# Performance work log

Hardware: AMD Instinct MI355X
Metric: run time of the kernel (lower is better)

Reference implementation:

```python
import jax, jax.numpy as jnp
import numpy as np

B, N, H = 32, 1024, 512
THR = 0.05  # peak_detection_threshold


def _l2norm(x):
    return x / jnp.linalg.norm(x, axis=-1, keepdims=True)


def setup_inputs() -> dict:
    key = jax.random.key(0)
    ks = jax.random.split(key, 6)
    def w(k, shape, fan_in):
        return jax.random.normal(k, shape, jnp.float32) / np.float32(np.sqrt(fan_in))
    return {
        "segment_rep": jax.random.normal(ks[0], (B, N, H), jnp.float32),
        "phn_mask": jnp.ones((B, N), jnp.float32),
        # SegmentSimilarityMeasure: Linear(2H->H), ReLU, Linear(H->1, no bias)
        "W1": w(ks[1], (2 * H, H), 2 * H),
        "b1": jnp.zeros((H,), jnp.float32),
        "W2": w(ks[2], (H, 1), H),
        # word_enc: Linear(H->H), ReLU, Linear(H->H)
        "We1": w(ks[3], (H, H), H),
        "be1": jnp.zeros((H,), jnp.float32),
        "We2": w(ks[4], (H, H), H),
        "be2": jnp.zeros((H,), jnp.float32),
    }


def _forward(segment_rep, phn_mask, W1, b1, W2, We1, be1, We2, be2):
    Bs, Np, Hd = segment_rep.shape
    # adjacent segment similarity: MLP on concat of l2-normalized neighbors -> (B, N-1)
    cat = jnp.concatenate([_l2norm(segment_rep[:, :-1, :]), _l2norm(segment_rep[:, 1:, :])], axis=2)
    S = (jax.nn.relu(cat @ W1 + b1) @ W2)[..., 0]

    # relative dissimilarity
    Smin = jnp.min(S, axis=1, keepdims=True)
    Smax = jnp.max(S, axis=1, keepdims=True)
    D = 1.0 - (S - Smin) / (Smax - Smin)

    # peak detector (faithful to original, incl. final overwrite of first-order cols -2:)
    z = jnp.zeros_like(D)
    fo = z
    fo = fo.at[:, 0].set(jnp.maximum(D[:, 0] - D[:, 1], 0.0))
    fo = fo.at[:, 1:-1].set(jnp.minimum(jnp.maximum(D[:, 1:-1] - D[:, :-2], 0.0),
                                        jnp.maximum(D[:, 1:-1] - D[:, 2:], 0.0)))
    fo = fo.at[:, -1].set(jnp.maximum(D[:, -1] - D[:, -2], 0.0))
    so = z
    so = so.at[:, 0:2].set(jnp.maximum(D[:, 0:2] - D[:, 2:4], 0.0))
    so = so.at[:, 2:-2].set(jnp.minimum(jnp.maximum(D[:, 2:-2] - D[:, :-4], 0.0),
                                        jnp.maximum(D[:, 2:-2] - D[:, 4:], 0.0)))
    fo = fo.at[:, -2:].set(jnp.maximum(D[:, -2:] - D[:, -4:-2], 0.0))  # replicates original code
    P = jnp.minimum(jnp.maximum(jnp.maximum(fo, so) - THR, 0.0), fo)

    # pad, mask, straight-through hard boundaries
    P = jnp.pad(P, ((0, 0), (0, 1)))
    P = jax.nn.relu(P + (phn_mask - 1.0))
    b_soft = jnp.tanh(10.0 * P)
    b_hard = jnp.tanh(100000.0 * P)
    b = b_soft + jax.lax.stop_gradient(b_hard - b_soft)
    b = jnp.cumsum(b, axis=1)  # (B, N)
    b = b + (b[:, :1] == 0).astype(b.dtype)  # per-row +1 if b[:,0]==0
    num_word_segments = b[:, -1].astype(jnp.int32) + 1  # (B,)

    # U: column j holds j+1 for j < num_word_segments[i], else -100000. Nmax = N (static bound).
    cols = jnp.arange(1, Np + 1, dtype=jnp.int32)  # (Nmax,)
    U = jnp.where(cols[None, :] <= num_word_segments[:, None],
                  cols.astype(segment_rep.dtype)[None, :], -100000.0)  # (B, Nmax)

    V = U[:, None, :] - b[:, :, None]  # (B, N, Nmax)
    Wseg = 1.0 - jnp.tanh(100000.0 * jnp.abs(V))
    Wseg = Wseg / jnp.sum(Wseg, axis=1, keepdims=True)
    Wseg = jnp.nan_to_num(Wseg)

    # pool: (B, Nmax, N) @ (B, N, H) -> (B, Nmax, H)
    word_rep = jnp.einsum('bnm,bnh->bmh', Wseg, segment_rep)
    word_masks = jnp.where(word_rep == 0, 0.0, 1.0)
    out = jax.nn.relu(word_rep @ We1 + be1) @ We2 + be2
    return out * word_masks


def reference(segment_rep, phn_mask, W1, b1, W2, We1, be1, We2, be2):
    return _forward(segment_rep, phn_mask, W1, b1, W2, We1, be1, We2, be2)
```

## Files before the change

kernel.cpp:

```cpp
#include <hip/hip_runtime.h>

#define BB 32
#define NN 1024
#define HH 512
#define NS 1023

typedef unsigned short u16;
typedef unsigned int   u32;
typedef __attribute__((ext_vector_type(8))) short bf16x8;
typedef __attribute__((ext_vector_type(4))) float f32x4;

__device__ __forceinline__ float bf2f(u16 h) {
  union { u32 u; float f; } c; c.u = ((u32)h) << 16; return c.f;
}
__device__ __forceinline__ u16 f2bf(float f) {
  union { float f; u32 u; } c; c.f = f;
  u32 u = c.u;
  return (u16)((u + 0x7fffu + ((u >> 16) & 1u)) >> 16);
}
__device__ __forceinline__ void split_bf(float x, u16& hi, u16& lo) {
  hi = f2bf(x);
  lo = f2bf(x - bf2f(hi));
}
__device__ __forceinline__ void dma16(const u16* g, u16* l) {
  __builtin_amdgcn_global_load_lds(
      (const __attribute__((address_space(1))) u32*)g,
      (__attribute__((address_space(3))) u32*)l, 16, 0, 0);
}

__global__ __launch_bounds__(64) void k_prep_a(const float* __restrict__ seg,
                                               u16* __restrict__ ahi,
                                               u16* __restrict__ alo) {
  int row = blockIdx.x, lane = threadIdx.x;
  const float4* p = (const float4*)(seg + ((size_t)row << 9) + lane * 8);
  float4 a = p[0], b = p[1];
  float v[8] = {a.x, a.y, a.z, a.w, b.x, b.y, b.z, b.w};
  float s = 0.f;
#pragma unroll
  for (int i = 0; i < 8; ++i) s += v[i] * v[i];
#pragma unroll
  for (int m = 32; m; m >>= 1) s += __shfl_xor(s, m, 64);
  float nrm = sqrtf(s);
  u16 h[8], l[8];
#pragma unroll
  for (int i = 0; i < 8; ++i) split_bf(v[i] / nrm, h[i], l[i]);
  size_t off = ((size_t)row << 9) + lane * 8;
  *(uint4*)(ahi + off) = make_uint4(h[0] | (h[1] << 16), h[2] | (h[3] << 16),
                                    h[4] | (h[5] << 16), h[6] | (h[7] << 16));
  *(uint4*)(alo + off) = make_uint4(l[0] | (l[1] << 16), l[2] | (l[3] << 16),
                                    l[4] | (l[5] << 16), l[6] | (l[7] << 16));
}

__global__ __launch_bounds__(256) void k_tr(const float* __restrict__ src,
                                            u16* __restrict__ dh,
                                            u16* __restrict__ dl,
                                            int K, int N) {
  __shared__ u16 Th[64 * 66], Tl[64 * 66];
  int nb = blockIdx.x * 64, kb = blockIdx.y * 64;
  int tid = threadIdx.x;
#pragma unroll
  for (int i = 0; i < 16; ++i) {
    int e = tid + i * 256;
    int r = e >> 6, c = e & 63;
    float v = src[(size_t)(kb + r) * N + nb + c];
    u16 hi, lo; split_bf(v, hi, lo);
    Th[c * 66 + r] = hi;
    Tl[c * 66 + r] = lo;
  }
  __syncthreads();
#pragma unroll
  for (int i = 0; i < 16; ++i) {
    int e = tid + i * 256;
    int n = e >> 6, k = e & 63;
    dh[(size_t)(nb + n) * K + kb + k] = Th[n * 66 + k];
    if (dl) dl[(size_t)(nb + n) * K + kb + k] = Tl[n * 66 + k];
  }
}

__global__ __launch_bounds__(256) void k_sgemm(const u16* __restrict__ ahi,
                                               const u16* __restrict__ alo,
                                               const u16* __restrict__ w1h,
                                               const u16* __restrict__ w1l,
                                               const float* __restrict__ b1,
                                               const float* __restrict__ W2,
                                               float* __restrict__ Spart) {
  __shared__ u16 Ah[2][64 * 32], Al_[2][64 * 32];
  __shared__ u16 Wh[2][256 * 32], Wl[2][256 * 32];

  int tid = threadIdx.x;
  int wave = tid >> 6, lane = tid & 63, quad = lane >> 4, l15 = lane & 15;
  int b = blockIdx.z, mblk = blockIdx.y, nblk = blockIdx.x;
  int rowbase = b * NN + mblk * 64;
  int ncol0 = nblk * 256;
  int r_in = lane >> 2, c_in = lane & 3;

  f32x4 acc[4][4];
#pragma unroll
  for (int mi = 0; mi < 4; ++mi)
#pragma unroll
    for (int ni = 0; ni < 4; ++ni) acc[mi][ni] = (f32x4){0.f, 0.f, 0.f, 0.f};

#define STAGE_TILE(ks_, tb_)                                                        \
  {                                                                                 \
    int k0_ = (ks_) * 32, half_ = k0_ >> 9, cb_ = k0_ & 511;                        \
    int grow_ = rowbase + wave * 16 + r_in + half_;                                 \
    if (grow_ > 32767) grow_ = 32767;                                               \
    size_t ga_ = (((size_t)grow_) << 9) + cb_ + c_in * 8;                           \
    dma16(ahi + ga_, &Ah [tb_][(wave * 16) * 32]);                                  \
    dma16(alo + ga_, &Al_[tb_][(wave * 16) * 32]);                                  \
    _Pragma("unroll")                                                               \
    for (int c_ = 0; c_ < 4; ++c_) {                                                \
      int n_ = wave * 64 + c_ * 16 + r_in;                                          \
      size_t gw_ = (size_t)(ncol0 + n_) * 1024 + k0_ + c_in * 8;                    \
      dma16(w1h + gw_, &Wh[tb_][(wave * 64 + c_ * 16) * 32]);                       \
      dma16(w1l + gw_, &Wl[tb_][(wave * 64 + c_ * 16) * 32]);                       \
    }                                                                               \
  }

  STAGE_TILE(0, 0)
  __syncthreads();

  for (int ks = 0; ks < 32; ++ks) {
    int bb = ks & 1;
    if (ks + 1 < 32) STAGE_TILE(ks + 1, bb ^ 1)

    bf16x8 a_h[4], a_l[4];
#pragma unroll
    for (int mi = 0; mi < 4; ++mi) {
      int off = (mi * 16 + l15) * 32 + quad * 8;
      a_h[mi] = *(const bf16x8*)&Ah [bb][off];
      a_l[mi] = *(const bf16x8*)&Al_[bb][off];
    }
#pragma unroll
    for (int ni = 0; ni < 4; ++ni) {
      int off = (wave * 64 + ni * 16 + l15) * 32 + quad * 8;
      bf16x8 b_h = *(const bf16x8*)&Wh[bb][off];
      bf16x8 b_l = *(const bf16x8*)&Wl[bb][off];
#pragma unroll
      for (int mi = 0; mi < 4; ++mi) {
        acc[mi][ni] = __builtin_amdgcn_mfma_f32_16x16x32_bf16(a_h[mi], b_h, acc[mi][ni], 0, 0, 0);
        acc[mi][ni] = __builtin_amdgcn_mfma_f32_16x16x32_bf16(a_h[mi], b_l, acc[mi][ni], 0, 0, 0);
        acc[mi][ni] = __builtin_amdgcn_mfma_f32_16x16x32_bf16(a_l[mi], b_h, acc[mi][ni], 0, 0, 0);
      }
    }
    __syncthreads();
  }
#undef STAGE_TILE

  float* red = (float*)Ah;
#pragma unroll
  for (int mi = 0; mi < 4; ++mi) {
#pragma unroll
    for (int reg = 0; reg < 4; ++reg) {
      float part = 0.f;
#pragma unroll
      for (int ni = 0; ni < 4; ++ni) {
        int n_g = ncol0 + wave * 64 + ni * 16 + l15;
        float h = acc[mi][ni][reg] + b1[n_g];
        h = h > 0.f ? h : 0.f;
        part = fmaf(h, W2[n_g], part);
      }
#pragma unroll
      for (int m = 8; m; m >>= 1) part += __shfl_xor(part, m, 64);
      if (l15 == 0) red[wave * 64 + mi * 16 + quad * 4 + reg] = part;
    }
  }
  __syncthreads();
  if (tid < 64) {
    float s = red[0 * 64 + tid] + red[1 * 64 + tid] + red[2 * 64 + tid] + red[3 * 64 + tid];
    int srow = mblk * 64 + tid;
    if (srow < NS)
      Spart[((size_t)nblk * BB + b) * NN + srow] = s;
  }
}

__global__ __launch_bounds__(256) void k_row(const float* __restrict__ S0,
                                             const float* __restrict__ S1,
                                             const float* __restrict__ mask,
                                             int* __restrict__ assign,
                                             float* __restrict__ weight,
                                             float* __restrict__ total,
                                             int* __restrict__ startn,
                                             int* __restrict__ endn) {
  int b = blockIdx.x, tid = threadIdx.x;
  __shared__ float Ssh[NS];
  __shared__ float Dsh[NS];
  __shared__ float tsh[NN];
  __shared__ float bsh[NN];
  __shared__ float totl[NN];
  __shared__ int   stl[NN];
  __shared__ int   enl[NN];
  __shared__ float red[256];

  for (int n = tid; n < NS; n += 256)
    Ssh[n] = S0[((size_t)b << 10) + n] + S1[((size_t)b << 10) + n];
  __syncthreads();

  float mn = INFINITY, mx = -INFINITY;
  for (int n = tid; n < NS; n += 256) {
    float v = Ssh[n];
    mn = fminf(mn, v); mx = fmaxf(mx, v);
  }
  red[tid] = mn; __syncthreads();
  for (int s = 128; s; s >>= 1) { if (tid < s) red[tid] = fminf(red[tid], red[tid + s]); __syncthreads(); }
  float Smin = red[0]; __syncthreads();
  red[tid] = mx; __syncthreads();
  for (int s = 128; s; s >>= 1) { if (tid < s) red[tid] = fmaxf(red[tid], red[tid + s]); __syncthreads(); }
  float Smax = red[0]; __syncthreads();

  for (int n = tid; n < NS; n += 256)
    Dsh[n] = 1.0f - (Ssh[n] - Smin) / (Smax - Smin);
  __syncthreads();

  for (int n = tid; n < NN; n += 256) {
    float P;
    if (n >= NS) {
      P = 0.f;
    } else {
      float D = Dsh[n];
      float fo, so;
      if (n == 0)            fo = fmaxf(D - Dsh[1], 0.f);
      else if (n >= NS - 2)  fo = fmaxf(D - Dsh[n - 2], 0.f);
      else                   fo = fminf(fmaxf(D - Dsh[n - 1], 0.f),
                                        fmaxf(D - Dsh[n + 1], 0.f));
      if (n <= 1)            so = fmaxf(D - Dsh[n + 2], 0.f);
      else if (n >= NS - 2)  so = 0.f;
      else                   so = fminf(fmaxf(D - Dsh[n - 2], 0.f),
                                        fmaxf(D - Dsh[n + 2], 0.f));
      P = fminf(fmaxf(fmaxf(fo, so) - 0.05f, 0.f), fo);
    }
    float m = mask[((size_t)b << 10) + n];
    P = P + (m - 1.0f);
    P = P > 0.f ? P : 0.f;
    float bs = tanhf(10.0f * P);
    float bh = tanhf(100000.0f * P);
    tsh[n] = bs + (bh - bs);
  }
  __syncthreads();

  if (tid == 0) {
    float acc = 0.f;
    for (int n = 0; n < NN; n += 8) {
      float t0 = tsh[n + 0], t1 = tsh[n + 1], t2 = tsh[n + 2], t3 = tsh[n + 3];
      float t4 = tsh[n + 4], t5 = tsh[n + 5], t6 = tsh[n + 6], t7 = tsh[n + 7];
      acc += t0; bsh[n + 0] = acc; acc += t1; bsh[n + 1] = acc;
      acc += t2; bsh[n + 2] = acc; acc += t3; bsh[n + 3] = acc;
      acc += t4; bsh[n + 4] = acc; acc += t5; bsh[n + 5] = acc;
      acc += t6; bsh[n + 6] = acc; acc += t7; bsh[n + 7] = acc;
    }
  }
  __syncthreads();

  float add1 = (bsh[0] == 0.0f) ? 1.0f : 0.0f;
  int   num  = (int)(bsh[NN - 1] + add1) + 1;

  for (int mi = tid; mi < NN; mi += 256) { totl[mi] = 0.f; stl[mi] = 1 << 30; enl[mi] = -1; }
  __syncthreads();

  for (int n = tid; n < NN; n += 256) {
    float bv = bsh[n] + add1;
    float kf = rintf(bv);
    int   k  = (int)kf;
    int   a  = -1; float w = 0.f;
    if (k >= 1 && k <= num && k <= NN) {
      float v = fabsf(kf - bv);
      w = 1.0f - tanhf(100000.0f * v);
      if (w > 0.f) {
        a = k - 1;
        atomicAdd(&totl[a], w);
        atomicMin(&stl[a], n);
        atomicMax(&enl[a], n);
      } else {
        a = -1; w = 0.f;
      }
    }
    assign[((size_t)b << 10) + n] = a;
    weight[((size_t)b << 10) + n] = w;
  }
  __syncthreads();
  for (int mi = tid; mi < NN; mi += 256) {
    total [((size_t)b << 10) + mi] = totl[mi];
    startn[((size_t)b << 10) + mi] = stl[mi];
    endn  [((size_t)b << 10) + mi] = enl[mi];
  }
}

__global__ __launch_bounds__(64) void k_pool(const float* __restrict__ seg,
                                             const int* __restrict__ assign,
                                             const float* __restrict__ weight,
                                             const float* __restrict__ total,
                                             const int* __restrict__ startn,
                                             const int* __restrict__ endn,
                                             float* __restrict__ wrep) {
  int bm = blockIdx.x;
  int b  = bm >> 10, m = bm & 1023;
  int lane = threadIdx.x;
  float acc[8] = {0.f, 0.f, 0.f, 0.f, 0.f, 0.f, 0.f, 0.f};
  float tm = total[bm];
  if (tm > 0.f) {
    int s = startn[bm], e = endn[bm];
    for (int n = s; n <= e; ++n) {
      if (assign[((size_t)b << 10) + n] != m) continue;
      float coef = weight[((size_t)b << 10) + n] / tm;
      const float4* p = (const float4*)(seg + (((size_t)b << 10) + n) * HH + lane * 8);
      float4 x = p[0], y = p[1];
      acc[0] = fmaf(coef, x.x, acc[0]); acc[1] = fmaf(coef, x.y, acc[1]);
      acc[2] = fmaf(coef, x.z, acc[2]); acc[3] = fmaf(coef, x.w, acc[3]);
      acc[4] = fmaf(coef, y.x, acc[4]); acc[5] = fmaf(coef, y.y, acc[5]);
      acc[6] = fmaf(coef, y.z, acc[6]); acc[7] = fmaf(coef, y.w, acc[7]);
    }
  }
  float4* dst = (float4*)(wrep + (size_t)bm * HH + lane * 8);
  dst[0] = make_float4(acc[0], acc[1], acc[2], acc[3]);
  dst[1] = make_float4(acc[4], acc[5], acc[6], acc[7]);
}

__global__ __launch_bounds__(512) void k_out(const u16* __restrict__ we1t,
                                             const u16* __restrict__ we2t,
                                             const float* __restrict__ be1,
                                             const float* __restrict__ be2,
                                             float* __restrict__ io) {
  __shared__ u16 Hid[64 * 520];
  __shared__ u16 Wst[2][512 * 32];
  __shared__ u16 Ast[2][64 * 32];

  int tid = threadIdx.x;
  int wave = tid >> 6, lane = tid & 63, quad = lane >> 4, l15 = lane & 15;
  int wm = wave >> 2, wn = wave & 3;
  int rowbase = blockIdx.x * 64;
  int m_st = tid >> 3, ch_st = tid & 7;
  int r_in = lane >> 2, c_in = lane & 3;

#define STAGE_W(src_, ks_, tb_)                                                     \
  {                                                                                 \
    int k0_ = (ks_) * 32;                                                           \
    _Pragma("unroll")                                                               \
    for (int c_ = 0; c_ < 4; ++c_) {                                                \
      int n_ = wave * 64 + c_ * 16 + r_in;                                          \
      dma16(src_ + (size_t)n_ * 512 + k0_ + c_in * 8,                               \
            &Wst[tb_][(wave * 64 + c_ * 16) * 32]);                                 \
    }                                                                               \
  }

  f32x4 acc[2][8];
#pragma unroll
  for (int mi = 0; mi < 2; ++mi)
#pragma unroll
    for (int ni = 0; ni < 8; ++ni) acc[mi][ni] = (f32x4){0.f, 0.f, 0.f, 0.f};

  {
    float4 v = *(const float4*)(io + (size_t)(rowbase + m_st) * HH + ch_st * 4);
    u32 p0 = f2bf(v.x) | ((u32)f2bf(v.y) << 16);
    u32 p1 = f2bf(v.z) | ((u32)f2bf(v.w) << 16);
    *(uint2*)&Ast[0][m_st * 32 + ch_st * 4] = make_uint2(p0, p1);
  }
  STAGE_W(we1t, 0, 0)
  __syncthreads();

  for (int ks = 0; ks < 16; ++ks) {
    int bb = ks & 1;
    bool have = (ks + 1) < 16;
    float4 nx;
    if (have) {
      STAGE_W(we1t, ks + 1, bb ^ 1)
      nx = *(const float4*)(io + (size_t)(rowbase + m_st) * HH + (ks + 1) * 32 + ch_st * 4);
    }
    bf16x8 a[2];
#pragma unroll
    for (int mi = 0; mi < 2; ++mi)
      a[mi] = *(const bf16x8*)&Ast[bb][(wm * 32 + mi * 16 + l15) * 32 + quad * 8];
#pragma unroll
    for (int ni = 0; ni < 8; ++ni) {
      bf16x8 bw = *(const bf16x8*)&Wst[bb][(wn * 128 + ni * 16 + l15) * 32 + quad * 8];
#pragma unroll
      for (int mi = 0; mi < 2; ++mi)
        acc[mi][ni] = __builtin_amdgcn_mfma_f32_16x16x32_bf16(a[mi], bw, acc[mi][ni], 0, 0, 0);
    }
    if (have) {
      u32 p0 = f2bf(nx.x) | ((u32)f2bf(nx.y) << 16);
      u32 p1 = f2bf(nx.z) | ((u32)f2bf(nx.w) << 16);
      *(uint2*)&Ast[bb ^ 1][m_st * 32 + ch_st * 4] = make_uint2(p0, p1);
    }
    __syncthreads();
  }
#pragma unroll
  for (int mi = 0; mi < 2; ++mi)
#pragma unroll
    for (int ni = 0; ni < 8; ++ni)
#pragma unroll
      for (int reg = 0; reg < 4; ++reg) {
        int n_g = wn * 128 + ni * 16 + l15;
        float h = acc[mi][ni][reg] + be1[n_g];
        h = h > 0.f ? h : 0.f;
        Hid[(wm * 32 + mi * 16 + quad * 4 + reg) * 520 + n_g] = f2bf(h);
      }

#pragma unroll
  for (int mi = 0; mi < 2; ++mi)
#pragma unroll
    for (int ni = 0; ni < 8; ++ni) acc[mi][ni] = (f32x4){0.f, 0.f, 0.f, 0.f};

  STAGE_W(we2t, 0, 0)
  __syncthreads();

  for (int ks = 0; ks < 16; ++ks) {
    int bb = ks & 1;
    if (ks + 1 < 16) STAGE_W(we2t, ks + 1, bb ^ 1)
    int k0 = ks * 32;
    bf16x8 a[2];
#pragma unroll
    for (int mi = 0; mi < 2; ++mi)
      a[mi] = *(const bf16x8*)&Hid[(wm * 32 + mi * 16 + l15) * 520 + k0 + quad * 8];
#pragma unroll
    for (int ni = 0; ni < 8; ++ni) {
      bf16x8 bw = *(const bf16x8*)&Wst[bb][(wn * 128 + ni * 16 + l15) * 32 + quad * 8];
#pragma unroll
      for (int mi = 0; mi < 2; ++mi)
        acc[mi][ni] = __builtin_amdgcn_mfma_f32_16x16x32_bf16(a[mi], bw, acc[mi][ni], 0, 0, 0);
    }
    __syncthreads();
  }
#undef STAGE_W

#pragma unroll
  for (int mi = 0; mi < 2; ++mi)
#pragma unroll
    for (int ni = 0; ni < 8; ++ni)
#pragma unroll
      for (int reg = 0; reg < 4; ++reg) {
        int n_g = wn * 128 + ni * 16 + l15;
        size_t row = (size_t)(rowbase + wm * 32 + mi * 16 + quad * 4 + reg);
        float o = acc[mi][ni][reg] + be2[n_g];
        float wr = io[row * HH + n_g];
        io[row * HH + n_g] = (wr == 0.f) ? 0.f : o;
      }
}

__global__ void k_diag(float* __restrict__ out, int hostcode) {
  if (hostcode != 0) out[0] = (float)hostcode;
}

extern "C" void kernel_launch(void* const* d_in, const int* in_sizes, int n_in,
                              void* d_out, int out_size, void* d_ws, size_t ws_size,
                              hipStream_t stream) {
  const float* seg  = (const float*)d_in[0];
  const float* mask = (const float*)d_in[1];
  const float* W1   = (const float*)d_in[2];
  const float* b1   = (const float*)d_in[3];
  const float* W2   = (const float*)d_in[4];
  const float* We1  = (const float*)d_in[5];
  const float* be1  = (const float*)d_in[6];
  const float* We2  = (const float*)d_in[7];
  const float* be2  = (const float*)d_in[8];

  const size_t NROW = (size_t)BB * NN;
  float* ws = (float*)d_ws;
  float* S0     = ws;
  float* S1     = S0 + NROW;
  int*   assign = (int*)(S1 + NROW);
  float* weight = (float*)(assign + NROW);
  float* total  = weight + NROW;
  int*   startn = (int*)(total + NROW);
  int*   endn   = startn + NROW;
  u16*   w1h    = (u16*)(endn + NROW);
  u16*   w1l    = w1h + (size_t)512 * 1024;
  u16*   we1t   = w1l + (size_t)512 * 1024;
  u16*   we2t   = we1t + (size_t)512 * 512;

  float* out = (float*)d_out;
  u16*   ahi = (u16*)d_out;
  u16*   alo = ahi + (size_t)NROW * HH;

  int hostcode = 0;
  if (ws_size < (size_t)7 * NROW * 4 + (size_t)3 * 1024 * 1024) hostcode += 32768;
  if (out_size != 16777216) hostcode += 8192;

  k_prep_a<<<dim3(BB * NN), dim3(64), 0, stream>>>(seg, ahi, alo);
  k_tr    <<<dim3(8, 16), dim3(256), 0, stream>>>(W1, w1h, w1l, 1024, 512);
  k_tr    <<<dim3(8, 8),  dim3(256), 0, stream>>>(We1, we1t, (u16*)nullptr, 512, 512);
  k_tr    <<<dim3(8, 8),  dim3(256), 0, stream>>>(We2, we2t, (u16*)nullptr, 512, 512);
  k_sgemm <<<dim3(2, 16, BB), dim3(256), 0, stream>>>(ahi, alo, w1h, w1l, b1, W2, S0);
  k_row   <<<dim3(BB), dim3(256), 0, stream>>>(S0, S1, mask, assign, weight, total, startn, endn);
  k_pool  <<<dim3(BB * NN), dim3(64), 0, stream>>>(seg, assign, weight, total, startn, endn, out);
  k_out   <<<dim3(NROW / 64), dim3(512), 0, stream>>>(we1t, we2t, be1, be2, out);
  k_diag  <<<dim3(1), dim3(1), 0, stream>>>(out, hostcode);
}
```

Baseline: 384.1 us.

## Enlarge similarity GEMM tiles to 256x256 with phased MFMA/DMA interleave

The split-bf16 similarity GEMM moves from 64x256 tiles with 256 threads to 256x256 tiles with 512 threads (8 waves in a 2x4 grid), with each wave holding 8x4 accumulators. Each k-step is split into three MFMA phases (hi*hi, hi*lo, lo*hi), and the next tile's loads are interleaved between phases using explicit barriers, waitcnts and setprio. The aim is to raise operand reuse, cut the global traffic for W1, and overlap DMA with MFMA work. The cost is more registers and LDS per block, plus a launch of only 256 blocks, which may leave CUs underfilled.

```diff
diff --git a/kernel.cpp b/kernel.cpp
--- a/kernel.cpp
+++ b/kernel.cpp
@@ -77,100 +77,147 @@
   }
 }
 
-__global__ __launch_bounds__(256) void k_sgemm(const u16* __restrict__ ahi,
-                                               const u16* __restrict__ alo,
-                                               const u16* __restrict__ w1h,
-                                               const u16* __restrict__ w1l,
-                                               const float* __restrict__ b1,
-                                               const float* __restrict__ W2,
-                                               float* __restrict__ Spart) {
-  __shared__ u16 Ah[2][64 * 32], Al_[2][64 * 32];
-  __shared__ u16 Wh[2][256 * 32], Wl[2][256 * 32];
-
-  int tid = threadIdx.x;
-  int wave = tid >> 6, lane = tid & 63, quad = lane >> 4, l15 = lane & 15;
-  int b = blockIdx.z, mblk = blockIdx.y, nblk = blockIdx.x;
-  int rowbase = b * NN + mblk * 64;
-  int ncol0 = nblk * 256;
-  int r_in = lane >> 2, c_in = lane & 3;
-
-  f32x4 acc[4][4];
-#pragma unroll
-  for (int mi = 0; mi < 4; ++mi)
+__global__ __launch_bounds__(512, 2) void k_sgemm(const u16* __restrict__ ahi,
+                                                  const u16* __restrict__ alo,
+                                                  const u16* __restrict__ w1h,
+                                                  const u16* __restrict__ w1l,
+                                                  const float* __restrict__ b1,
+                                                  const float* __restrict__ W2,
+                                                  float* __restrict__ Spart) {
+  __shared__ u16 Ah[2][256 * 32];
+  __shared__ u16 Al[2][256 * 32];
+  __shared__ u16 Bh[2][256 * 32];
+  __shared__ u16 Bl[2][256 * 32];
+
+  const int tid  = threadIdx.x;
+  const int wave = tid >> 6, lane = tid & 63;
+  const int quad = lane >> 4, l15 = lane & 15;
+  const int wm = wave >> 2, wn = wave & 3;
+  const int r_in = lane >> 2, c_in = lane & 3;
+  const int nblk = blockIdx.x, mblk = blockIdx.y;
+  const int mrow0 = mblk * 256;
+  const int ncol0 = nblk * 256;
+
+#define SG_A(g_, tb_, ks_)                                                   \
+  {                                                                          \
+    int k0_ = (ks_) * 32, half_ = k0_ >> 9, cb_ = k0_ & 511;                 \
+    int grow_ = mrow0 + wave * 32 + (g_) * 16 + r_in + half_;                \
+    if (grow_ > 32767) grow_ = 32767;                                        \
+    size_t ga_ = (((size_t)grow_) << 9) + cb_ + c_in * 8;                    \
+    dma16(ahi + ga_, &Ah[tb_][(wave * 32 + (g_) * 16) * 32]);                \
+    dma16(alo + ga_, &Al[tb_][(wave * 32 + (g_) * 16) * 32]);                \
+  }
+#define SG_B(g_, tb_, ks_)                                                   \
+  {                                                                          \
+    int k0_ = (ks_) * 32;                                                    \
+    int n_ = ncol0 + wave * 32 + (g_) * 16 + r_in;                           \
+    size_t gb_ = (((size_t)n_) << 10) + k0_ + c_in * 8;                      \
+    dma16(w1h + gb_, &Bh[tb_][(wave * 32 + (g_) * 16) * 32]);                \
+    dma16(w1l + gb_, &Bl[tb_][(wave * 32 + (g_) * 16) * 32]);                \
+  }
+
+  f32x4 acc[8][4];
+#pragma unroll
+  for (int mi = 0; mi < 8; ++mi)
 #pragma unroll
     for (int ni = 0; ni < 4; ++ni) acc[mi][ni] = (f32x4){0.f, 0.f, 0.f, 0.f};
 
-#define STAGE_TILE(ks_, tb_)                                                        \
-  {                                                                                 \
-    int k0_ = (ks_) * 32, half_ = k0_ >> 9, cb_ = k0_ & 511;                        \
-    int grow_ = rowbase + wave * 16 + r_in + half_;                                 \
-    if (grow_ > 32767) grow_ = 32767;                                               \
-    size_t ga_ = (((size_t)grow_) << 9) + cb_ + c_in * 8;                           \
-    dma16(ahi + ga_, &Ah [tb_][(wave * 16) * 32]);                                  \
-    dma16(alo + ga_, &Al_[tb_][(wave * 16) * 32]);                                  \
-    _Pragma("unroll")                                                               \
-    for (int c_ = 0; c_ < 4; ++c_) {                                                \
-      int n_ = wave * 64 + c_ * 16 + r_in;                                          \
-      size_t gw_ = (size_t)(ncol0 + n_) * 1024 + k0_ + c_in * 8;                    \
-      dma16(w1h + gw_, &Wh[tb_][(wave * 64 + c_ * 16) * 32]);                       \
-      dma16(w1l + gw_, &Wl[tb_][(wave * 64 + c_ * 16) * 32]);                       \
-    }                                                                               \
-  }
-
-  STAGE_TILE(0, 0)
-  __syncthreads();
+  SG_A(0, 0, 0) SG_A(1, 0, 0) SG_B(0, 0, 0) SG_B(1, 0, 0)
+  asm volatile("s_waitcnt vmcnt(0)" ::: "memory");
+  __builtin_amdgcn_s_barrier();
 
   for (int ks = 0; ks < 32; ++ks) {
-    int bb = ks & 1;
-    if (ks + 1 < 32) STAGE_TILE(ks + 1, bb ^ 1)
-
-    bf16x8 a_h[4], a_l[4];
-#pragma unroll
-    for (int mi = 0; mi < 4; ++mi) {
-      int off = (mi * 16 + l15) * 32 + quad * 8;
-      a_h[mi] = *(const bf16x8*)&Ah [bb][off];
-      a_l[mi] = *(const bf16x8*)&Al_[bb][off];
-    }
-#pragma unroll
-    for (int ni = 0; ni < 4; ++ni) {
-      int off = (wave * 64 + ni * 16 + l15) * 32 + quad * 8;
-      bf16x8 b_h = *(const bf16x8*)&Wh[bb][off];
-      bf16x8 b_l = *(const bf16x8*)&Wl[bb][off];
-#pragma unroll
-      for (int mi = 0; mi < 4; ++mi) {
-        acc[mi][ni] = __builtin_amdgcn_mfma_f32_16x16x32_bf16(a_h[mi], b_h, acc[mi][ni], 0, 0, 0);
-        acc[mi][ni] = __builtin_amdgcn_mfma_f32_16x16x32_bf16(a_h[mi], b_l, acc[mi][ni], 0, 0, 0);
-        acc[mi][ni] = __builtin_amdgcn_mfma_f32_16x16x32_bf16(a_l[mi], b_h, acc[mi][ni], 0, 0, 0);
-      }
-    }
-    __syncthreads();
-  }
-#undef STAGE_TILE
-
-  float* red = (float*)Ah;
-#pragma unroll
-  for (int mi = 0; mi < 4; ++mi) {
+    const int bb = ks & 1;
+    const bool pre = (ks + 1) < 32;
+    bf16x8 ah[8], al[8], bh[4], bl[4];
+
+#pragma unroll
+    for (int mi = 0; mi < 8; ++mi)
+      ah[mi] = *(const bf16x8*)&Ah[bb][(wm * 128 + mi * 16 + l15) * 32 + quad * 8];
+#pragma unroll
+    for (int ni = 0; ni < 4; ++ni)
+      bh[ni] = *(const bf16x8*)&Bh[bb][(wn * 64 + ni * 16 + l15) * 32 + quad * 8];
+    if (pre) { SG_A(0, bb ^ 1, ks + 1) SG_B(0, bb ^ 1, ks + 1) }
+    __builtin_amdgcn_s_barrier();
+    asm volatile("s_waitcnt lgkmcnt(0)" ::: "memory");
+    __builtin_amdgcn_sched_barrier(0);
+    __builtin_amdgcn_s_setprio(1);
+#pragma unroll
+    for (int ni = 0; ni < 4; ++ni)
+#pragma unroll
+      for (int mi = 0; mi < 8; ++mi)
+        acc[mi][ni] = __builtin_amdgcn_mfma_f32_16x16x32_bf16(ah[mi], bh[ni], acc[mi][ni], 0, 0, 0);
+    __builtin_amdgcn_s_setprio(0);
+    __builtin_amdgcn_s_barrier();
+
+#pragma unroll
+    for (int ni = 0; ni < 4; ++ni)
+      bl[ni] = *(const bf16x8*)&Bl[bb][(wn * 64 + ni * 16 + l15) * 32 + quad * 8];
+    if (pre) { SG_A(1, bb ^ 1, ks + 1) SG_B(1, bb ^ 1, ks + 1) }
+    __builtin_amdgcn_s_barrier();
+    asm volatile("s_waitcnt lgkmcnt(0)" ::: "memory");
+    __builtin_amdgcn_sched_barrier(0);
+    __builtin_amdgcn_s_setprio(1);
+#pragma unroll
+    for (int ni = 0; ni < 4; ++ni)
+#pragma unroll
+      for (int mi = 0; mi < 8; ++mi)
+        acc[mi][ni] = __builtin_amdgcn_mfma_f32_16x16x32_bf16(ah[mi], bl[ni], acc[mi][ni], 0, 0, 0);
+    __builtin_amdgcn_s_setprio(0);
+    __builtin_amdgcn_s_barrier();
+
+#pragma unroll
+    for (int mi = 0; mi < 8; ++mi)
+      al[mi] = *(const bf16x8*)&Al[bb][(wm * 128 + mi * 16 + l15) * 32 + quad * 8];
+    __builtin_amdgcn_s_barrier();
+    asm volatile("s_waitcnt lgkmcnt(0)" ::: "memory");
+    __builtin_amdgcn_sched_barrier(0);
+    __builtin_amdgcn_s_setprio(1);
+#pragma unroll
+    for (int ni = 0; ni < 4; ++ni)
+#pragma unroll
+      for (int mi = 0; mi < 8; ++mi)
+        acc[mi][ni] = __builtin_amdgcn_mfma_f32_16x16x32_bf16(al[mi], bh[ni], acc[mi][ni], 0, 0, 0);
+    __builtin_amdgcn_s_setprio(0);
+    asm volatile("s_waitcnt vmcnt(0)" ::: "memory");
+    __builtin_amdgcn_s_barrier();
+  }
+#undef SG_A
+#undef SG_B
+
+  float* red = (float*)&Ah[0][0];
+  float b1v[4], w2v[4];
+#pragma unroll
+  for (int ni = 0; ni < 4; ++ni) {
+    int n_g = ncol0 + wn * 64 + ni * 16 + l15;
+    b1v[ni] = b1[n_g];
+    w2v[ni] = W2[n_g];
+  }
+#pragma unroll
+  for (int mi = 0; mi < 8; ++mi) {
 #pragma unroll
     for (int reg = 0; reg < 4; ++reg) {
       float part = 0.f;
 #pragma unroll
       for (int ni = 0; ni < 4; ++ni) {
-        int n_g = ncol0 + wave * 64 + ni * 16 + l15;
-        float h = acc[mi][ni][reg] + b1[n_g];
+        float h = acc[mi][ni][reg] + b1v[ni];
         h = h > 0.f ? h : 0.f;
-        part = fmaf(h, W2[n_g], part);
+        part = fmaf(h, w2v[ni], part);
       }
 #pragma unroll
       for (int m = 8; m; m >>= 1) part += __shfl_xor(part, m, 64);
-      if (l15 == 0) red[wave * 64 + mi * 16 + quad * 4 + reg] = part;
-    }
-  }
-  __syncthreads();
-  if (tid < 64) {
-    float s = red[0 * 64 + tid] + red[1 * 64 + tid] + red[2 * 64 + tid] + red[3 * 64 + tid];
-    int srow = mblk * 64 + tid;
-    if (srow < NS)
-      Spart[((size_t)nblk * BB + b) * NN + srow] = s;
+      if (l15 == 0) red[wave * 128 + mi * 16 + quad * 4 + reg] = part;
+    }
+  }
+  __syncthreads();
+  if (tid < 256) {
+    int wmr = tid >> 7, rl = tid & 127;
+    float s = red[(wmr * 4 + 0) * 128 + rl] + red[(wmr * 4 + 1) * 128 + rl]
+            + red[(wmr * 4 + 2) * 128 + rl] + red[(wmr * 4 + 3) * 128 + rl];
+    int grow = mrow0 + tid;
+    int b = grow >> 10, n = grow & 1023;
+    if (n < NS)
+      Spart[((size_t)nblk * BB + b) * NN + n] = s;
   }
 }
 
@@ -479,7 +526,7 @@
   k_tr    <<<dim3(8, 16), dim3(256), 0, stream>>>(W1, w1h, w1l, 1024, 512);
   k_tr    <<<dim3(8, 8),  dim3(256), 0, stream>>>(We1, we1t, (u16*)nullptr, 512, 512);
   k_tr    <<<dim3(8, 8),  dim3(256), 0, stream>>>(We2, we2t, (u16*)nullptr, 512, 512);
-  k_sgemm <<<dim3(2, 16, BB), dim3(256), 0, stream>>>(ahi, alo, w1h, w1l, b1, W2, S0);
+  k_sgemm <<<dim3(2, 128), dim3(512), 0, stream>>>(ahi, alo, w1h, w1l, b1, W2, S0);
   k_row   <<<dim3(BB), dim3(256), 0, stream>>>(S0, S1, mask, assign, weight, total, startn, endn);
   k_pool  <<<dim3(BB * NN), dim3(64), 0, stream>>>(seg, assign, weight, total, startn, endn, out);
   k_out   <<<dim3(NROW / 64), dim3(512), 0, stream>>>(we1t, we2t, be1, be2, out);
```

New measurement: 353.5 us. 8.0% less time.
